# Kernel optimization log

Hardware: AMD Instinct MI355X
Metric: run time of the kernel (lower is better)

Reference implementation:

```python
import jax, jax.numpy as jnp
import numpy as np

N, C, S = 64, 128, 12          # batch, channels, input_size
HW = S * S                      # 144
RIN = S ** 4


def setup_inputs() -> dict:
    key = jax.random.key(0)
    ks = jax.random.split(key, 6)
    x1 = jax.random.normal(ks[0], (N, C, S, S), dtype=jnp.float32)
    x2 = jax.random.normal(ks[1], (N, C, S, S), dtype=jnp.float32)
    # Linear weights stored [in, out]; scaled ~1/sqrt(fan_in) like torch default
    w1 = jax.random.normal(ks[2], (RIN, RIN // 4), dtype=jnp.float32) / np.sqrt(RIN)
    w2 = jax.random.normal(ks[3], (RIN // 4, RIN // 16), dtype=jnp.float32) / np.sqrt(RIN // 4)
    w3 = jax.random.normal(ks[4], (RIN // 16, RIN // 64), dtype=jnp.float32) / np.sqrt(RIN // 16)
    w4 = jax.random.normal(ks[5], (RIN // 64, 8), dtype=jnp.float32) / np.sqrt(RIN // 64)
    return {
        "x1": x1, "x2": x2,
        "w1": w1, "b1": jnp.zeros((RIN // 4,), jnp.float32),
        "w2": w2, "b2": jnp.zeros((RIN // 16,), jnp.float32),
        "w3": w3, "b3": jnp.zeros((RIN // 64,), jnp.float32),
        "w4": w4, "b4": jnp.zeros((8,), jnp.float32),
    }


def _l2_normalize(x):
    # torch: norm over dim=1 (channels), broadcast divide -> per-(n,h,w) unit vectors
    return x / jnp.linalg.norm(x, axis=1, keepdims=True)


def reference(x1, x2, w1, b1, w2, b2, w3, b3, w4, b4):
    n, c, h, w = x1.shape
    x1n = _l2_normalize(x1)
    x2n = _l2_normalize(x2)
    # out[n, k, i, j] = sum_c x1n[n,c,i,j] * x2n_flat[n,c,k]  (k flattens x2's HxW)
    corr = jnp.einsum('ncij,nck->nkij', x1n, x2n.reshape(n, c, h * w))  # [N, HW, H, W]
    x = corr.reshape(n, h * w * h * w)  # [N, S^4]
    x = jax.nn.relu(x @ w1 + b1)
    x = jax.nn.relu(x @ w2 + b2)
    x = jnp.tanh(x @ w3 + b3)
    H = x @ w4 + b4  # [N, 8]
    ones = jnp.ones((n, 1), dtype=H.dtype)
    return jnp.concatenate([H, ones], axis=1).reshape(n, 3, 3)
```

## Files before the change

### kernel.cpp

```cpp
#include <hip/hip_runtime.h>
#include <stdint.h>
#include <math.h>


typedef short short8 __attribute__((ext_vector_type(8)));
typedef float f32x4 __attribute__((ext_vector_type(4)));

__device__ __forceinline__ unsigned bf16u(float x) {
    return (__float_as_uint(x) + 0x8000u) >> 16;
}
__device__ __forceinline__ unsigned packbf(float a, float b) {
    return ((__float_as_uint(a) + 0x8000u) >> 16) |
           ((__float_as_uint(b) + 0x8000u) & 0xFFFF0000u);
}
__device__ __forceinline__ float bf2f(unsigned short u) {
    return __uint_as_float(((unsigned)u) << 16);
}

__global__ __launch_bounds__(1024) void kcorr2(const float* __restrict__ x1,
                                               const float* __restrict__ x2,
                                               unsigned short* __restrict__ Abuf) {
    __shared__ unsigned short s1[144 * 136];
    __shared__ unsigned short s2[144 * 136];
    __shared__ float rn1[144], rn2[144];
    int n = blockIdx.x, t = threadIdx.x;
    const float* p1 = x1 + n * 18432;
    const float* p2 = x2 + n * 18432;
#pragma unroll
    for (int i = 0; i < 18; ++i) {
        int g = t + 1024 * i;
        int c = g / 144, ij = g - c * 144;
        s1[ij * 136 + c] = (unsigned short)bf16u(p1[g]);
        s2[ij * 136 + c] = (unsigned short)bf16u(p2[g]);
    }
    __syncthreads();
    if (t < 144) {
        float acc = 0.f;
        for (int c = 0; c < 128; ++c) { float v = bf2f(s1[t * 136 + c]); acc += v * v; }
        rn1[t] = 1.0f / sqrtf(acc);
    } else if (t < 288) {
        int ij = t - 144;
        float acc = 0.f;
        for (int c = 0; c < 128; ++c) { float v = bf2f(s2[ij * 136 + c]); acc += v * v; }
        rn2[ij] = 1.0f / sqrtf(acc);
    }
    __syncthreads();
    int lane = t & 63, w = t >> 6;
    int col = lane & 15, quad = lane >> 4;
    unsigned short* out = Abuf + n * 20736;
    for (int tt = w; tt < 81; tt += 16) {
        int m0 = (tt / 9) * 16, n0 = (tt % 9) * 16;
        f32x4 acc = {0.f, 0.f, 0.f, 0.f};
        const short8* a0 = (const short8*)(s2 + (m0 + col) * 136 + quad * 8);
        const short8* b0 = (const short8*)(s1 + (n0 + col) * 136 + quad * 8);
#pragma unroll
        for (int ks = 0; ks < 4; ++ks) {
            short8 a = a0[ks * 4];
            short8 bv = b0[ks * 4];
            acc = __builtin_amdgcn_mfma_f32_16x16x32_bf16(a, bv, acc, 0, 0, 0);
        }
        float rc = rn1[n0 + col];
#pragma unroll
        for (int r = 0; r < 4; ++r) {
            int row = m0 + quad * 4 + r;
            out[row * 144 + n0 + col] = (unsigned short)bf16u(acc[r] * rn2[row] * rc);
        }
    }
}

template <int N, int KTOT, int KCHUNK>
__global__ __launch_bounds__(256) void kgemm(const unsigned short* __restrict__ A,
                                             const float* __restrict__ W,
                                             float* __restrict__ Cf) {
    int lane = threadIdx.x & 63;
    int w = threadIdx.x >> 6;
    int col = lane & 15, quad = lane >> 4;
    int c0 = blockIdx.x * 64 + w * 16;
    int kc = blockIdx.y * KCHUNK;
    const unsigned short* Ap = A + kc + quad * 8;
    const float* Wp = W + (size_t)(kc + quad * 8) * N + c0 + col;
    f32x4 acc0 = {0, 0, 0, 0}, acc1 = {0, 0, 0, 0}, acc2 = {0, 0, 0, 0}, acc3 = {0, 0, 0, 0};
#pragma unroll 2
    for (int ks = 0; ks < KCHUNK / 32; ++ks) {
        int kk = ks * 32;
        short8 a0 = *(const short8*)(Ap + (0 * 16 + col) * KTOT + kk);
        short8 a1 = *(const short8*)(Ap + (1 * 16 + col) * KTOT + kk);
        short8 a2 = *(const short8*)(Ap + (2 * 16 + col) * KTOT + kk);
        short8 a3 = *(const short8*)(Ap + (3 * 16 + col) * KTOT + kk);
        const float* wp = Wp + (size_t)kk * N;
        float b0 = wp[0 * (size_t)N];
        float b1 = wp[1 * (size_t)N];
        float b2 = wp[2 * (size_t)N];
        float b3 = wp[3 * (size_t)N];
        float b4 = wp[4 * (size_t)N];
        float b5 = wp[5 * (size_t)N];
        float b6 = wp[6 * (size_t)N];
        float b7 = wp[7 * (size_t)N];
        union { unsigned u[4]; short8 s; } bu;
        bu.u[0] = packbf(b0, b1);
        bu.u[1] = packbf(b2, b3);
        bu.u[2] = packbf(b4, b5);
        bu.u[3] = packbf(b6, b7);
        acc0 = __builtin_amdgcn_mfma_f32_16x16x32_bf16(a0, bu.s, acc0, 0, 0, 0);
        acc1 = __builtin_amdgcn_mfma_f32_16x16x32_bf16(a1, bu.s, acc1, 0, 0, 0);
        acc2 = __builtin_amdgcn_mfma_f32_16x16x32_bf16(a2, bu.s, acc2, 0, 0, 0);
        acc3 = __builtin_amdgcn_mfma_f32_16x16x32_bf16(a3, bu.s, acc3, 0, 0, 0);
    }
#pragma unroll
    for (int r = 0; r < 4; ++r) {
        int row0 = quad * 4 + r;
        atomicAdd(&Cf[(0 * 16 + row0) * N + c0 + col], acc0[r]);
        atomicAdd(&Cf[(1 * 16 + row0) * N + c0 + col], acc1[r]);
        atomicAdd(&Cf[(2 * 16 + row0) * N + c0 + col], acc2[r]);
        atomicAdd(&Cf[(3 * 16 + row0) * N + c0 + col], acc3[r]);
    }
}

template <int N, int KTOT, int KCHUNK>
__global__ __launch_bounds__(256) void kgemm2f(const float* __restrict__ Af,
                                               const float* __restrict__ bias,
                                               const float* __restrict__ W,
                                               float* __restrict__ Cf) {
    int lane = threadIdx.x & 63;
    int w = threadIdx.x >> 6;
    int col = lane & 15, quad = lane >> 4;
    int c0 = blockIdx.x * 64 + w * 16;
    if (c0 >= N) return;
    int kc = blockIdx.y * KCHUNK;
    int kb = kc + quad * 8;
    const float* Ap = Af + kb;
    const float* Wp = W + (size_t)kb * N + c0 + col;
    f32x4 acc0 = {0, 0, 0, 0}, acc1 = {0, 0, 0, 0}, acc2 = {0, 0, 0, 0}, acc3 = {0, 0, 0, 0};
#pragma unroll 2
    for (int ks = 0; ks < KCHUNK / 32; ++ks) {
        int kk = ks * 32;
        f32x4 bb0 = *(const f32x4*)(bias + kb + kk);
        f32x4 bb1 = *(const f32x4*)(bias + kb + kk + 4);
        union { unsigned u[4]; short8 s; } au[4];
#pragma unroll
        for (int i = 0; i < 4; ++i) {
            const float* ap = Ap + (size_t)(i * 16 + col) * KTOT + kk;
            f32x4 v0 = *(const f32x4*)(ap);
            f32x4 v1 = *(const f32x4*)(ap + 4);
            float r0 = fmaxf(v0[0] + bb0[0], 0.f), r1 = fmaxf(v0[1] + bb0[1], 0.f);
            float r2 = fmaxf(v0[2] + bb0[2], 0.f), r3 = fmaxf(v0[3] + bb0[3], 0.f);
            float r4 = fmaxf(v1[0] + bb1[0], 0.f), r5 = fmaxf(v1[1] + bb1[1], 0.f);
            float r6 = fmaxf(v1[2] + bb1[2], 0.f), r7 = fmaxf(v1[3] + bb1[3], 0.f);
            au[i].u[0] = packbf(r0, r1); au[i].u[1] = packbf(r2, r3);
            au[i].u[2] = packbf(r4, r5); au[i].u[3] = packbf(r6, r7);
        }
        const float* wp = Wp + (size_t)kk * N;
        float b0 = wp[0 * (size_t)N];
        float b1 = wp[1 * (size_t)N];
        float b2 = wp[2 * (size_t)N];
        float b3 = wp[3 * (size_t)N];
        float b4 = wp[4 * (size_t)N];
        float b5 = wp[5 * (size_t)N];
        float b6 = wp[6 * (size_t)N];
        float b7 = wp[7 * (size_t)N];
        union { unsigned u[4]; short8 s; } bu;
        bu.u[0] = packbf(b0, b1);
        bu.u[1] = packbf(b2, b3);
        bu.u[2] = packbf(b4, b5);
        bu.u[3] = packbf(b6, b7);
        acc0 = __builtin_amdgcn_mfma_f32_16x16x32_bf16(au[0].s, bu.s, acc0, 0, 0, 0);
        acc1 = __builtin_amdgcn_mfma_f32_16x16x32_bf16(au[1].s, bu.s, acc1, 0, 0, 0);
        acc2 = __builtin_amdgcn_mfma_f32_16x16x32_bf16(au[2].s, bu.s, acc2, 0, 0, 0);
        acc3 = __builtin_amdgcn_mfma_f32_16x16x32_bf16(au[3].s, bu.s, acc3, 0, 0, 0);
    }
#pragma unroll
    for (int r = 0; r < 4; ++r) {
        int row0 = quad * 4 + r;
        atomicAdd(&Cf[(0 * 16 + row0) * N + c0 + col], acc0[r]);
        atomicAdd(&Cf[(1 * 16 + row0) * N + c0 + col], acc1[r]);
        atomicAdd(&Cf[(2 * 16 + row0) * N + c0 + col], acc2[r]);
        atomicAdd(&Cf[(3 * 16 + row0) * N + c0 + col], acc3[r]);
    }
}

__global__ __launch_bounds__(384) void kgemm3(const float* __restrict__ C2f,
                                              const float* __restrict__ b2,
                                              const float* __restrict__ W3,
                                              float* __restrict__ C3f) {
    __shared__ float as[324];
    int n = blockIdx.x, sl = blockIdx.y;
    int t = threadIdx.x;
    if (t < 324) as[t] = fmaxf(C2f[n * 1296 + sl * 324 + t] + b2[sl * 324 + t], 0.f);
    __syncthreads();
    if (t < 324) {
        float acc = 0.f;
        const float* wp = W3 + sl * 324 * 324 + t;
#pragma unroll 4
        for (int k = 0; k < 324; ++k) acc += as[k] * wp[k * 324];
        atomicAdd(&C3f[n * 324 + t], acc);
    }
}

__global__ __launch_bounds__(384) void kep3g4(const float* __restrict__ C3f,
                                              const float* __restrict__ b3,
                                              const float* __restrict__ W4,
                                              const float* __restrict__ b4,
                                              float* __restrict__ out) {
    __shared__ float t3[324];
    int n = blockIdx.x, t = threadIdx.x;
    if (t < 324) t3[t] = tanhf(C3f[n * 324 + t] + b3[t]);
    __syncthreads();
    if (t < 8) {
        float acc = b4[t];
        for (int k = 0; k < 324; ++k) acc += t3[k] * W4[k * 8 + t];
        out[n * 9 + t] = acc;
    } else if (t == 8) {
        out[n * 9 + 8] = 1.0f;
    }
}

extern "C" void kernel_launch(void* const* d_in, const int* in_sizes, int n_in,
                              void* d_out, int out_size, void* d_ws, size_t ws_size,
                              hipStream_t stream) {
    const float* x1 = (const float*)d_in[0];
    const float* x2 = (const float*)d_in[1];
    const float* w1 = (const float*)d_in[2];
    const float* b1 = (const float*)d_in[3];
    const float* w2 = (const float*)d_in[4];
    const float* b2 = (const float*)d_in[5];
    const float* w3 = (const float*)d_in[6];
    const float* b3 = (const float*)d_in[7];
    const float* w4 = (const float*)d_in[8];
    const float* b4 = (const float*)d_in[9];
    float* out = (float*)d_out;

    char* ws = (char*)d_ws;
    unsigned short* Abuf = (unsigned short*)(ws + 0);
    float* C1f = (float*)(ws + 2654208);
    float* C2f = (float*)(ws + 3981312);
    float* C3f = (float*)(ws + 4313088);

    hipMemsetAsync(ws + 2654208, 0, 1741824, stream);
    kcorr2<<<64, 1024, 0, stream>>>(x1, x2, Abuf);
    kgemm<5184, 20736, 2592><<<dim3(81, 8), 256, 0, stream>>>(Abuf, w1, C1f);
    kgemm2f<1296, 5184, 288><<<dim3(21, 18), 256, 0, stream>>>(C1f, b1, w2, C2f);
    kgemm3<<<dim3(64, 4), 384, 0, stream>>>(C2f, b2, w3, C3f);
    kep3g4<<<64, 384, 0, stream>>>(C3f, b3, w4, b4, out);
}
```

Before: 750.5 us.

## Split all stages across more blocks for higher GPU occupancy

The correlation kernel is split three ways per batch over x2 rows. The three GEMM stages get more split-K chunks (more grid blocks, more atomics). The final epilogue uses 64 threads with vectorized W4 loads and a shared-memory reduction instead of an 8-thread serial loop. The aim is to fill more of the GPU's compute units in each small launch, at the cost of redundant x1 loading and normalization per split and more atomic traffic.

```diff
diff --git a/kernel.cpp b/kernel.cpp
--- a/kernel.cpp
+++ b/kernel.cpp
@@ -21,9 +21,11 @@
                                                const float* __restrict__ x2,
                                                unsigned short* __restrict__ Abuf) {
     __shared__ unsigned short s1[144 * 136];
-    __shared__ unsigned short s2[144 * 136];
-    __shared__ float rn1[144], rn2[144];
-    int n = blockIdx.x, t = threadIdx.x;
+    __shared__ unsigned short s2p[48 * 136];
+    __shared__ float rn1[144], rn2p[48];
+    int b = blockIdx.x;
+    int n = b / 3, p = b - n * 3;
+    int t = threadIdx.x;
     const float* p1 = x1 + n * 18432;
     const float* p2 = x2 + n * 18432;
 #pragma unroll
@@ -31,27 +33,32 @@
         int g = t + 1024 * i;
         int c = g / 144, ij = g - c * 144;
         s1[ij * 136 + c] = (unsigned short)bf16u(p1[g]);
-        s2[ij * 136 + c] = (unsigned short)bf16u(p2[g]);
+    }
+#pragma unroll
+    for (int i = 0; i < 6; ++i) {
+        int g = t + 1024 * i;
+        int c = g / 48, ijl = g - c * 48;
+        s2p[ijl * 136 + c] = (unsigned short)bf16u(p2[c * 144 + p * 48 + ijl]);
     }
     __syncthreads();
     if (t < 144) {
         float acc = 0.f;
         for (int c = 0; c < 128; ++c) { float v = bf2f(s1[t * 136 + c]); acc += v * v; }
         rn1[t] = 1.0f / sqrtf(acc);
-    } else if (t < 288) {
-        int ij = t - 144;
+    } else if (t < 192) {
+        int ijl = t - 144;
         float acc = 0.f;
-        for (int c = 0; c < 128; ++c) { float v = bf2f(s2[ij * 136 + c]); acc += v * v; }
-        rn2[ij] = 1.0f / sqrtf(acc);
+        for (int c = 0; c < 128; ++c) { float v = bf2f(s2p[ijl * 136 + c]); acc += v * v; }
+        rn2p[ijl] = 1.0f / sqrtf(acc);
     }
     __syncthreads();
     int lane = t & 63, w = t >> 6;
     int col = lane & 15, quad = lane >> 4;
-    unsigned short* out = Abuf + n * 20736;
-    for (int tt = w; tt < 81; tt += 16) {
-        int m0 = (tt / 9) * 16, n0 = (tt % 9) * 16;
+    unsigned short* out = Abuf + n * 20736 + p * 48 * 144;
+    for (int tt = w; tt < 27; tt += 16) {
+        int ml0 = (tt / 9) * 16, n0 = (tt % 9) * 16;
         f32x4 acc = {0.f, 0.f, 0.f, 0.f};
-        const short8* a0 = (const short8*)(s2 + (m0 + col) * 136 + quad * 8);
+        const short8* a0 = (const short8*)(s2p + (ml0 + col) * 136 + quad * 8);
         const short8* b0 = (const short8*)(s1 + (n0 + col) * 136 + quad * 8);
 #pragma unroll
         for (int ks = 0; ks < 4; ++ks) {
@@ -62,8 +69,8 @@
         float rc = rn1[n0 + col];
 #pragma unroll
         for (int r = 0; r < 4; ++r) {
-            int row = m0 + quad * 4 + r;
-            out[row * 144 + n0 + col] = (unsigned short)bf16u(acc[r] * rn2[row] * rc);
+            int rl = ml0 + quad * 4 + r;
+            out[rl * 144 + n0 + col] = (unsigned short)bf16u(acc[r] * rn2p[rl] * rc);
         }
     }
 }
@@ -182,32 +189,55 @@
                                               const float* __restrict__ b2,
                                               const float* __restrict__ W3,
                                               float* __restrict__ C3f) {
-    __shared__ float as[324];
+    __shared__ float as[162];
     int n = blockIdx.x, sl = blockIdx.y;
     int t = threadIdx.x;
-    if (t < 324) as[t] = fmaxf(C2f[n * 1296 + sl * 324 + t] + b2[sl * 324 + t], 0.f);
+    int base = sl * 162;
+    if (t < 162) as[t] = fmaxf(C2f[n * 1296 + base + t] + b2[base + t], 0.f);
     __syncthreads();
     if (t < 324) {
         float acc = 0.f;
-        const float* wp = W3 + sl * 324 * 324 + t;
-#pragma unroll 4
-        for (int k = 0; k < 324; ++k) acc += as[k] * wp[k * 324];
+        const float* wp = W3 + (size_t)base * 324 + t;
+#pragma unroll 6
+        for (int k = 0; k < 162; ++k) acc += as[k] * wp[k * 324];
         atomicAdd(&C3f[n * 324 + t], acc);
     }
 }
 
-__global__ __launch_bounds__(384) void kep3g4(const float* __restrict__ C3f,
+__global__ __launch_bounds__(128) void kep3g4(const float* __restrict__ C3f,
                                               const float* __restrict__ b3,
                                               const float* __restrict__ W4,
                                               const float* __restrict__ b4,
                                               float* __restrict__ out) {
     __shared__ float t3[324];
+    __shared__ float part[64][8];
     int n = blockIdx.x, t = threadIdx.x;
-    if (t < 324) t3[t] = tanhf(C3f[n * 324 + t] + b3[t]);
+    for (int i = t; i < 324; i += 128) t3[i] = tanhf(C3f[n * 324 + i] + b3[i]);
+    __syncthreads();
+    if (t < 64) {
+        float acc[8];
+#pragma unroll
+        for (int j = 0; j < 8; ++j) acc[j] = 0.f;
+#pragma unroll
+        for (int kk = 0; kk < 6; ++kk) {
+            int k = t + 64 * kk;
+            if (k < 324) {
+                float v = t3[k];
+                f32x4 w0 = *(const f32x4*)(W4 + k * 8);
+                f32x4 w1 = *(const f32x4*)(W4 + k * 8 + 4);
+                acc[0] += v * w0[0]; acc[1] += v * w0[1];
+                acc[2] += v * w0[2]; acc[3] += v * w0[3];
+                acc[4] += v * w1[0]; acc[5] += v * w1[1];
+                acc[6] += v * w1[2]; acc[7] += v * w1[3];
+            }
+        }
+#pragma unroll
+        for (int j = 0; j < 8; ++j) part[t][j] = acc[j];
+    }
     __syncthreads();
     if (t < 8) {
         float acc = b4[t];
-        for (int k = 0; k < 324; ++k) acc += t3[k] * W4[k * 8 + t];
+        for (int l = 0; l < 64; ++l) acc += part[l][t];
         out[n * 9 + t] = acc;
     } else if (t == 8) {
         out[n * 9 + 8] = 1.0f;
@@ -236,9 +266,9 @@
     float* C3f = (float*)(ws + 4313088);
 
     hipMemsetAsync(ws + 2654208, 0, 1741824, stream);
-    kcorr2<<<64, 1024, 0, stream>>>(x1, x2, Abuf);
-    kgemm<5184, 20736, 2592><<<dim3(81, 8), 256, 0, stream>>>(Abuf, w1, C1f);
-    kgemm2f<1296, 5184, 288><<<dim3(21, 18), 256, 0, stream>>>(C1f, b1, w2, C2f);
-    kgemm3<<<dim3(64, 4), 384, 0, stream>>>(C2f, b2, w3, C3f);
-    kep3g4<<<64, 384, 0, stream>>>(C3f, b3, w4, b4, out);
-}
+    kcorr2<<<192, 1024, 0, stream>>>(x1, x2, Abuf);
+    kgemm<5184, 20736, 1152><<<dim3(81, 18), 256, 0, stream>>>(Abuf, w1, C1f);
+    kgemm2f<1296, 5184, 192><<<dim3(21, 27), 256, 0, stream>>>(C1f, b1, w2, C2f);
+    kgemm3<<<dim3(64, 8), 384, 0, stream>>>(C2f, b2, w3, C3f);
+    kep3g4<<<64, 128, 0, stream>>>(C3f, b3, w4, b4, out);
+}
```

Measured after the change: 679.6 us. -9.5%, faster.
